# Performance work log

Measured on AMD Instinct MI355X. Metric: run time of the kernel, lower is better.

Reference implementation:

```python
import jax, jax.numpy as jnp
import numpy as np
from jax.ops import segment_sum

N_NODE, N_EDGE, D_IN, D_HID, N_CLS = 50000, 800000, 64, 64, 40


def setup_inputs() -> dict:
    key = jax.random.key(0)
    k1, k2, k3, k4 = jax.random.split(key, 4)
    x = jax.random.normal(k1, (N_NODE, D_IN), dtype=jnp.float32)
    edge_index = jax.random.randint(k2, (2, N_EDGE), 0, N_NODE, dtype=jnp.int64)
    W1 = jax.random.normal(k3, (D_IN, D_HID), dtype=jnp.float32) * (1.0 / np.sqrt(D_IN))
    b1 = jnp.zeros((D_HID,), dtype=jnp.float32)
    W2 = jax.random.normal(k4, (D_HID, N_CLS), dtype=jnp.float32) * (1.0 / np.sqrt(D_HID))
    b2 = jnp.zeros((N_CLS,), dtype=jnp.float32)
    return {"x": x, "edge_index": edge_index, "W1": W1, "b1": b1, "W2": W2, "b2": b2}


def _att_weights(fea, row, col, n):
    # edge-parallel cosine similarity (sklearn cosine_similarity restricted to edges)
    nrm = jnp.sqrt(jnp.sum(fea * fea, axis=1, keepdims=True))
    fn = fea / jnp.maximum(nrm, 1e-12)
    sim = jnp.sum(fn[row] * fn[col], axis=1)                 # [E]
    sim = jnp.where(sim < 0.1, 0.0, sim)                      # threshold
    # L1 row-normalization (sim >= 0 after threshold)
    rs = segment_sum(sim, row, num_segments=n)                # [N]
    sim_n = jnp.where(sim > 0, sim / jnp.maximum(rs[row], 1e-12), 0.0)
    # degree-based self-loop weight lam = 1/(deg+1)
    deg = segment_sum((sim > 0).astype(fea.dtype), row, num_segments=n)
    lam = 1.0 / (deg + 1.0)
    # exp applied only to stored (nonzero) entries; zeroed edges stay 0
    w_edge = jnp.where(sim > 0, jnp.exp(sim_n), 0.0)          # [E]
    w_self = jnp.exp(lam)                                     # [N] self-loop weights
    return w_edge, w_self


def _gcn(h, W, b, row, col, w_edge, w_self, n):
    # symmetric-norm GCN over weighted edges + explicit self loops
    deg = segment_sum(w_edge, row, num_segments=n) + w_self
    dinv = 1.0 / jnp.sqrt(jnp.maximum(deg, 1e-12))
    h = h @ W                                                 # [N, F]
    coef = w_edge * dinv[row] * dinv[col]                     # [E]
    out = segment_sum(coef[:, None] * h[col], row, num_segments=n)
    out = out + (w_self * dinv * dinv)[:, None] * h + b
    return out


def reference(x, edge_index, W1, b1, W2, b2):
    n = x.shape[0]
    row, col = edge_index[0], edge_index[1]
    # layer 1: attention coefs from raw features
    w1e, w1s = _att_weights(x, row, col, n)
    h = jax.nn.relu(_gcn(x, W1, b1, row, col, w1e, w1s, n))
    # layer 2: attention coefs recomputed on hidden features (dropout = eval mode)
    w2e, w2s = _att_weights(h, row, col, n)
    out = _gcn(h, W2, b2, row, col, w2e, w2s, n)
    return jax.nn.log_softmax(out, axis=1)
```

## Files before the change

### kernel.cpp

```cpp
#include <hip/hip_runtime.h>
#include <math.h>


#define ATT_CAP 96
#define EPB     2048
#define RPB     128
#define NBUCK_MAX 512
#define CAPB    4096

typedef _Float16 half4 __attribute__((ext_vector_type(4)));

__global__ void k_normfn(const float* __restrict__ fea, float* __restrict__ fn, int n)
{
    int gid  = blockIdx.x * blockDim.x + threadIdx.x;
    int wid  = gid >> 6;
    int lane = threadIdx.x & 63;
    if (wid >= n) return;
    float v = fea[(size_t)wid * 64 + lane];
    float s = v * v;
#pragma unroll
    for (int off = 32; off > 0; off >>= 1) s += __shfl_xor(s, off);
    float inv = 1.0f / fmaxf(sqrtf(s), 1e-12f);
    fn[(size_t)wid * 64 + lane] = v * inv;
}

__global__ void k_bhist(const int* __restrict__ row, int* __restrict__ hist,
                        int* __restrict__ btot, int E, int nblkA, int nbuck)
{
    __shared__ int lh[NBUCK_MAX];
    int b = blockIdx.x;
    int ebeg = b * EPB, eend = ebeg + EPB; if (eend > E) eend = E;
    for (int i = threadIdx.x; i < nbuck; i += blockDim.x) lh[i] = 0;
    __syncthreads();
    for (int e = ebeg + threadIdx.x; e < eend; e += blockDim.x)
        atomicAdd(&lh[row[e] >> 7], 1);
    __syncthreads();
    for (int i = threadIdx.x; i < nbuck; i += blockDim.x) {
        int c = lh[i];
        hist[(size_t)i * nblkA + b] = c;
        if (c) atomicAdd(btot + i, c);
    }
}

__global__ void k_bscan(const int* __restrict__ btot, int* __restrict__ bbase, int nbuck)
{
    int lane = threadIdx.x;
    int K = (nbuck + 63) / 64;
    int beg = lane * K;
    int s = 0;
    for (int i = 0; i < K; ++i) { int idx = beg + i; if (idx < nbuck) s += btot[idx]; }
    int incl = s;
#pragma unroll
    for (int off = 1; off < 64; off <<= 1) {
        int v = __shfl_up(incl, off);
        if (lane >= off) incl += v;
    }
    int run = incl - s;
    for (int i = 0; i < K; ++i) {
        int idx = beg + i;
        if (idx < nbuck) { bbase[idx] = run; run += btot[idx]; }
    }
    if (lane == 63) bbase[nbuck] = incl;
}

__global__ void k_mscan(int* __restrict__ hist, const int* __restrict__ bbase,
                        int nbuck, int nblkA)
{
    int wib  = threadIdx.x >> 6;
    int j    = blockIdx.x * 4 + wib;
    int lane = threadIdx.x & 63;
    if (j >= nbuck) return;
    int run = bbase[j];
    size_t base = (size_t)j * nblkA;
    for (int b0 = 0; b0 < nblkA; b0 += 64) {
        int b = b0 + lane;
        int v = (b < nblkA) ? hist[base + b] : 0;
        int incl = v;
#pragma unroll
        for (int off = 1; off < 64; off <<= 1) {
            int t = __shfl_up(incl, off);
            if (lane >= off) incl += t;
        }
        if (b < nblkA) hist[base + b] = run + (incl - v);
        run += __shfl(incl, 63);
    }
}

__global__ void k_bscat(const int* __restrict__ row, const int* __restrict__ col,
                        const int* __restrict__ hist, int* __restrict__ ebuf,
                        int E, int nblkA, int nbuck)
{
    __shared__ int lh[NBUCK_MAX];
    int b = blockIdx.x;
    int ebeg = b * EPB, eend = ebeg + EPB; if (eend > E) eend = E;
    for (int i = threadIdx.x; i < nbuck; i += blockDim.x)
        lh[i] = hist[(size_t)i * nblkA + b];
    __syncthreads();
    for (int e = ebeg + threadIdx.x; e < eend; e += blockDim.x) {
        int r = row[e];
        int j = r >> 7;
        int pos = atomicAdd(&lh[j], 1);
        ebuf[pos] = ((r & (RPB - 1)) << 16) | col[e];
    }
}

__global__ void k_csr(const int* __restrict__ ebuf, const int* __restrict__ bbase,
                      int* __restrict__ rptr, int* __restrict__ col_s, int N, int E)
{
    __shared__ int pk[CAPB];
    __shared__ int lcol[CAPB];
    __shared__ int lcnt[RPB], lexc[RPB], lcur[RPB];
    int j = blockIdx.x;
    int beg = bbase[j], end = bbase[j + 1];
    int m = end - beg; if (m > CAPB) m = CAPB;
    int tid = threadIdx.x;
    for (int i = tid; i < m; i += blockDim.x) pk[i] = ebuf[beg + i];
    if (tid < RPB) lcnt[tid] = 0;
    __syncthreads();
    for (int i = tid; i < m; i += blockDim.x) atomicAdd(&lcnt[pk[i] >> 16], 1);
    __syncthreads();
    if (tid < 64) {
        int a = lcnt[2 * tid], b2 = lcnt[2 * tid + 1];
        int s = a + b2;
        int incl = s;
#pragma unroll
        for (int off = 1; off < 64; off <<= 1) {
            int v = __shfl_up(incl, off);
            if (tid >= off) incl += v;
        }
        int base = incl - s;
        lexc[2 * tid] = base;     lexc[2 * tid + 1] = base + a;
        lcur[2 * tid] = base;     lcur[2 * tid + 1] = base + a;
    }
    __syncthreads();
    for (int i = tid; i < m; i += blockDim.x) {
        int v = pk[i];
        int p = atomicAdd(&lcur[v >> 16], 1);
        lcol[p] = v & 0xFFFF;
    }
    __syncthreads();
    for (int i = tid; i < m; i += blockDim.x) col_s[beg + i] = lcol[i];
    if (tid < RPB) {
        int r = j * RPB + tid;
        if (r < N) rptr[r] = beg + lexc[tid];
    }
    if (j == 0 && tid == 0) rptr[N] = E;
}

__global__ void k_att(const float* __restrict__ fn,
                      const int* __restrict__ rptr, const int* __restrict__ col_s,
                      int2* __restrict__ cw, int* __restrict__ lend,
                      float* __restrict__ dinv, float* __restrict__ selfc, int n)
{
    __shared__ float ssim[4][ATT_CAP];
    __shared__ int   scol[4][ATT_CAP];
    int wib  = threadIdx.x >> 6;
    int wid  = blockIdx.x * 4 + wib;
    int lane = threadIdx.x & 63;
    if (wid >= n) return;
    int sub = lane & 7;
    int grp = lane >> 3;
    int beg = rptr[wid], end = rptr[wid + 1];
    int deg_all = end - beg;

    const float4* frp = (const float4*)(fn + (size_t)wid * 64);
    float4 a0 = frp[sub * 2], a1 = frp[sub * 2 + 1];

    float rs_part = 0.0f;
    int ngrp = (deg_all + 7) >> 3;
    for (int g = 0; g < ngrp; ++g) {
        int li = g * 8 + grp;
        float s = 0.0f; int c = 0;
        bool valid = (li < deg_all);
        if (valid) {
            c = col_s[beg + li];
            const float4* fcp = (const float4*)(fn + (size_t)c * 64);
            float4 b0 = fcp[sub * 2], b1 = fcp[sub * 2 + 1];
            float p = a0.x * b0.x + a0.y * b0.y + a0.z * b0.z + a0.w * b0.w
                    + a1.x * b1.x + a1.y * b1.y + a1.z * b1.z + a1.w * b1.w;
            p += __shfl_xor(p, 1);
            p += __shfl_xor(p, 2);
            p += __shfl_xor(p, 4);
            s = (p < 0.1f) ? 0.0f : p;
        }
        if (sub == 0 && valid) {
            if (li < ATT_CAP) { ssim[wib][li] = s; scol[wib][li] = c; }
            if (s > 0.0f) rs_part += s;
        }
    }
#pragma unroll
    for (int off = 32; off > 0; off >>= 1) rs_part += __shfl_xor(rs_part, off);
    float denom = fmaxf(rs_part, 1e-12f);

    int   nlive = 0;
    float sw_lane = 0.0f;
    for (int base = 0; base < deg_all; base += 64) {
        int li = base + lane;
        bool valid = (li < deg_all);
        float s = 0.0f; int c = 0;
        if (valid) {
            if (li < ATT_CAP) { s = ssim[wib][li]; c = scol[wib][li]; }
            else {
                c = col_s[beg + li];
                const float* fr = fn + (size_t)wid * 64;
                const float* fc = fn + (size_t)c * 64;
                float p = 0.0f;
                for (int k = 0; k < 64; ++k) p += fr[k] * fc[k];
                s = (p < 0.1f) ? 0.0f : p;
            }
        }
        float w = (valid && s > 0.0f) ? expf(s / denom) : 0.0f;
        unsigned long long M = __ballot(w > 0.0f);
        int rank = __popcll(M & ((1ull << lane) - 1ull));
        if (w > 0.0f) {
            int2 pw; pw.x = c; pw.y = __float_as_int(w);
            cw[beg + nlive + rank] = pw;
            sw_lane += w;
        }
        nlive += __popcll(M);
    }
#pragma unroll
    for (int off = 32; off > 0; off >>= 1) sw_lane += __shfl_xor(sw_lane, off);

    if (lane == 0) {
        float wself = expf(1.0f / ((float)nlive + 1.0f));
        float D  = sw_lane + wself;
        float di = rsqrtf(fmaxf(D, 1e-12f));
        lend[wid]  = beg + nlive;
        dinv[wid]  = di;
        selfc[wid] = wself * di;
    }
}

template <int F, typename InT>
__global__ void k_gemm(const InT* __restrict__ fea, const float* __restrict__ W,
                       const float* __restrict__ scale, _Float16* __restrict__ out, int n)
{
    constexpr int R = 256 / F;
    __shared__ float sW[64 * F];
    __shared__ float sX[R * 64];
    int tid = threadIdx.x;
    for (int i = tid; i < 64 * F; i += 256) sW[i] = W[i];
    int base = blockIdx.x * R;
    for (int i = tid; i < R * 64; i += 256) {
        int rr = base + i / 64;
        sX[i] = (rr < n) ? (float)fea[(size_t)rr * 64 + (i & 63)] : 0.0f;
    }
    __syncthreads();
    int rl = tid / F, j = tid % F;
    if (rl >= R) return;
    int r = base + rl;
    if (r >= n) return;
    float acc = 0.0f;
#pragma unroll
    for (int k = 0; k < 64; ++k) acc = fmaf(sX[rl * 64 + k], sW[k * F + j], acc);
    out[(size_t)r * F + j] = (_Float16)(acc * scale[r]);
}

template <int F>
__device__ inline float agg_core_t(const _Float16* __restrict__ hd,
                                   const int2* __restrict__ cw,
                                   int beg, int lend_, int lane)
{
    int q  = lane & 15;
    int eg = lane >> 4;
    bool qact = (F == 64) ? true : (q < (F >> 2));
    float acc0 = 0.f, acc1 = 0.f, acc2 = 0.f, acc3 = 0.f;
    for (int base = beg; base < lend_; base += 64) {
        int idx = base + lane;
        int cv = 0; float wv = 0.0f;
        if (idx < lend_) { int2 pw = cw[idx]; cv = pw.x; wv = __int_as_float(pw.y); }
        int cnt = lend_ - base; if (cnt > 64) cnt = 64;
        for (int j = 0; j < cnt; j += 4) {
            int   c = __shfl(cv, j + eg);
            float w = __shfl(wv, j + eg);
            if (qact) {
                half4 hv = *(const half4*)(hd + (size_t)c * F + q * 4);
                acc0 += w * (float)hv.x;
                acc1 += w * (float)hv.y;
                acc2 += w * (float)hv.z;
                acc3 += w * (float)hv.w;
            }
        }
    }
    acc0 += __shfl_xor(acc0, 16); acc0 += __shfl_xor(acc0, 32);
    acc1 += __shfl_xor(acc1, 16); acc1 += __shfl_xor(acc1, 32);
    acc2 += __shfl_xor(acc2, 16); acc2 += __shfl_xor(acc2, 32);
    acc3 += __shfl_xor(acc3, 16); acc3 += __shfl_xor(acc3, 32);
    int srcq = lane >> 2;
    float a0 = __shfl(acc0, srcq);
    float a1 = __shfl(acc1, srcq);
    float a2 = __shfl(acc2, srcq);
    float a3 = __shfl(acc3, srcq);
    int k = lane & 3;
    return (k == 0) ? a0 : (k == 1) ? a1 : (k == 2) ? a2 : a3;
}

__global__ void k_agg64(const _Float16* __restrict__ hd, const int2* __restrict__ cw,
                        const float* __restrict__ dinv, const float* __restrict__ selfc,
                        const float* __restrict__ b, const int* __restrict__ row_ptr,
                        const int* __restrict__ lend,
                        _Float16* __restrict__ hrelu16, float* __restrict__ fnh, int n)
{
    int gid  = blockIdx.x * blockDim.x + threadIdx.x;
    int wid  = gid >> 6;
    int lane = threadIdx.x & 63;
    if (wid >= n) return;
    int beg = row_ptr[wid], le = lend[wid];
    float accf = agg_core_t<64>(hd, cw, beg, le, lane);
    float hs  = (float)hd[(size_t)wid * 64 + lane];
    float v = dinv[wid] * accf + selfc[wid] * hs + b[lane];
    v = fmaxf(v, 0.0f);
    hrelu16[(size_t)wid * 64 + lane] = (_Float16)v;
    float s = v * v;
#pragma unroll
    for (int off = 32; off > 0; off >>= 1) s += __shfl_xor(s, off);
    float inv = 1.0f / fmaxf(sqrtf(s), 1e-12f);
    fnh[(size_t)wid * 64 + lane] = v * inv;
}

__global__ void k_agg40_lsm(const _Float16* __restrict__ hd2, const int2* __restrict__ cw,
                            const float* __restrict__ dinv, const float* __restrict__ selfc,
                            const float* __restrict__ b, const int* __restrict__ row_ptr,
                            const int* __restrict__ lend,
                            float* __restrict__ out, int n)
{
    constexpr int F = 40;
    int gid  = blockIdx.x * blockDim.x + threadIdx.x;
    int wid  = gid >> 6;
    int lane = threadIdx.x & 63;
    if (wid >= n) return;
    int beg = row_ptr[wid], le = lend[wid];
    float accf = agg_core_t<F>(hd2, cw, beg, le, lane);
    bool active = (lane < F);
    float v = 0.0f;
    if (active) {
        float hs = (float)hd2[(size_t)wid * F + lane];
        v = dinv[wid] * accf + selfc[wid] * hs + b[lane];
    }
    float m = active ? v : -__builtin_inff();
#pragma unroll
    for (int off = 32; off > 0; off >>= 1) m = fmaxf(m, __shfl_xor(m, off));
    float ex = active ? expf(v - m) : 0.0f;
    float s = ex;
#pragma unroll
    for (int off = 32; off > 0; off >>= 1) s += __shfl_xor(s, off);
    if (active) out[(size_t)wid * F + lane] = v - m - logf(s);
}

extern "C" void kernel_launch(void* const* d_in, const int* in_sizes, int n_in,
                              void* d_out, int out_size, void* d_ws, size_t ws_size,
                              hipStream_t stream)
{
    const float* x  = (const float*)d_in[0];
    const int*   ei = (const int*)d_in[1];
    const float* W1 = (const float*)d_in[2];
    const float* b1 = (const float*)d_in[3];
    const float* W2 = (const float*)d_in[4];
    const float* b2 = (const float*)d_in[5];
    float* out = (float*)d_out;

    const int N = in_sizes[0] / 64;
    const int E = in_sizes[1] / 2;
    const int* row = ei;
    const int* col = ei + E;

    const int nblkA = (E + EPB - 1) / EPB;
    const int nbuck = (N + RPB - 1) / RPB;

    char* p = (char*)d_ws;
    auto alloc = [&](size_t bytes) -> char* {
        char* r = p; p += (bytes + 255) & ~(size_t)255; return r;
    };
    float*     fn     = (float*)alloc((size_t)N * 64 * 4);
    float*     dinv   = (float*)alloc((size_t)N * 4);
    float*     selfc  = (float*)alloc((size_t)N * 4);
    _Float16*  hd1    = (_Float16*)alloc((size_t)N * 64 * 2);
    _Float16*  hrelu  = (_Float16*)alloc((size_t)N * 64 * 2);
    _Float16*  hd2    = (_Float16*)alloc((size_t)N * 40 * 2);
    float*     fnh    = (float*)alloc((size_t)N * 64 * 4);
    int*       rptr   = (int*)alloc((size_t)(N + 1) * 4);
    int*       lendv  = (int*)alloc((size_t)N * 4);
    int*       col_s  = (int*)alloc((size_t)E * 4);
    int2*      cw     = (int2*)alloc((size_t)E * 8);
    int*       ebuf   = (int*)alloc((size_t)E * 4);
    int*       hist   = (int*)alloc((size_t)nbuck * nblkA * 4);
    int*       btot   = (int*)alloc((size_t)nbuck * 4);
    int*       bbase  = (int*)alloc((size_t)(nbuck + 1) * 4);

    const int TB = 256;
    int blk_nodeWave = (N * 64 + TB - 1) / TB;
    int blk_node4    = (N + 3) / 4;

    hipMemsetAsync(btot, 0, (size_t)nbuck * 4, stream);

    k_bhist<<<nblkA, TB, 0, stream>>>(row, hist, btot, E, nblkA, nbuck);
    k_bscan<<<1, 64, 0, stream>>>(btot, bbase, nbuck);
    k_mscan<<<(nbuck + 3) / 4, TB, 0, stream>>>(hist, bbase, nbuck, nblkA);
    k_bscat<<<nblkA, TB, 0, stream>>>(row, col, hist, ebuf, E, nblkA, nbuck);
    k_csr<<<nbuck, TB, 0, stream>>>(ebuf, bbase, rptr, col_s, N, E);

    k_normfn<<<blk_nodeWave, TB, 0, stream>>>(x, fn, N);
    k_att<<<blk_node4, TB, 0, stream>>>(fn, rptr, col_s, cw, lendv, dinv, selfc, N);
    k_gemm<64, float><<<(N + 3) / 4, TB, 0, stream>>>(x, W1, dinv, hd1, N);
    k_agg64<<<blk_nodeWave, TB, 0, stream>>>(hd1, cw, dinv, selfc, b1,
                                             rptr, lendv, hrelu, fnh, N);

    k_att<<<blk_node4, TB, 0, stream>>>(fnh, rptr, col_s, cw, lendv, dinv, selfc, N);
    k_gemm<40, _Float16><<<(N + 5) / 6, TB, 0, stream>>>(hrelu, W2, dinv, hd2, N);
    k_agg40_lsm<<<blk_nodeWave, TB, 0, stream>>>(hd2, cw, dinv, selfc, b2,
                                                 rptr, lendv, out, N);
}
```

Before: 285.5 us.

## Replace per-block histogram scan with atomic bucket cursors; store layer-1 features in fp32

The bucket sort no longer writes a per-block histogram matrix and drops the multi-block scan kernel. Each scatter block now counts its edges locally, reserves a contiguous range per bucket with one global atomicAdd on a cursor array, and writes its edges in a second pass from registers. This removes one kernel launch and the histogram traffic, at the cost of a nondeterministic edge order inside each bucket, which the CSR pass later sorts by row. Separately, the layer-1 transformed features are now kept in fp32 rather than fp16. That doubles the gather bytes in the first aggregation but removes the fp16 conversion error.

```diff
diff --git a/kernel.cpp b/kernel.cpp
--- a/kernel.cpp
+++ b/kernel.cpp
@@ -24,8 +24,8 @@
     fn[(size_t)wid * 64 + lane] = v * inv;
 }
 
-__global__ void k_bhist(const int* __restrict__ row, int* __restrict__ hist,
-                        int* __restrict__ btot, int E, int nblkA, int nbuck)
+__global__ void k_bhist(const int* __restrict__ row, int* __restrict__ btot,
+                        int E, int nbuck)
 {
     __shared__ int lh[NBUCK_MAX];
     int b = blockIdx.x;
@@ -35,14 +35,12 @@
     for (int e = ebeg + threadIdx.x; e < eend; e += blockDim.x)
         atomicAdd(&lh[row[e] >> 7], 1);
     __syncthreads();
-    for (int i = threadIdx.x; i < nbuck; i += blockDim.x) {
-        int c = lh[i];
-        hist[(size_t)i * nblkA + b] = c;
-        if (c) atomicAdd(btot + i, c);
-    }
-}
-
-__global__ void k_bscan(const int* __restrict__ btot, int* __restrict__ bbase, int nbuck)
+    for (int i = threadIdx.x; i < nbuck; i += blockDim.x)
+        if (lh[i]) atomicAdd(btot + i, lh[i]);
+}
+
+__global__ void k_bscan(const int* __restrict__ btot, int* __restrict__ bbase,
+                        int* __restrict__ gcur, int nbuck)
 {
     int lane = threadIdx.x;
     int K = (nbuck + 63) / 64;
@@ -58,49 +56,38 @@
     int run = incl - s;
     for (int i = 0; i < K; ++i) {
         int idx = beg + i;
-        if (idx < nbuck) { bbase[idx] = run; run += btot[idx]; }
+        if (idx < nbuck) { bbase[idx] = run; gcur[idx] = run; run += btot[idx]; }
     }
     if (lane == 63) bbase[nbuck] = incl;
 }
 
-__global__ void k_mscan(int* __restrict__ hist, const int* __restrict__ bbase,
-                        int nbuck, int nblkA)
-{
-    int wib  = threadIdx.x >> 6;
-    int j    = blockIdx.x * 4 + wib;
-    int lane = threadIdx.x & 63;
-    if (j >= nbuck) return;
-    int run = bbase[j];
-    size_t base = (size_t)j * nblkA;
-    for (int b0 = 0; b0 < nblkA; b0 += 64) {
-        int b = b0 + lane;
-        int v = (b < nblkA) ? hist[base + b] : 0;
-        int incl = v;
-#pragma unroll
-        for (int off = 1; off < 64; off <<= 1) {
-            int t = __shfl_up(incl, off);
-            if (lane >= off) incl += t;
-        }
-        if (b < nblkA) hist[base + b] = run + (incl - v);
-        run += __shfl(incl, 63);
-    }
-}
-
 __global__ void k_bscat(const int* __restrict__ row, const int* __restrict__ col,
-                        const int* __restrict__ hist, int* __restrict__ ebuf,
-                        int E, int nblkA, int nbuck)
+                        int* __restrict__ gcur, int* __restrict__ ebuf, int E, int nbuck)
 {
     __shared__ int lh[NBUCK_MAX];
+    __shared__ int lbase[NBUCK_MAX];
     int b = blockIdx.x;
     int ebeg = b * EPB, eend = ebeg + EPB; if (eend > E) eend = E;
-    for (int i = threadIdx.x; i < nbuck; i += blockDim.x)
-        lh[i] = hist[(size_t)i * nblkA + b];
+    int rr[8], cc[8];
+    int ne = 0;
+    for (int i = threadIdx.x; i < nbuck; i += blockDim.x) lh[i] = 0;
     __syncthreads();
     for (int e = ebeg + threadIdx.x; e < eend; e += blockDim.x) {
-        int r = row[e];
-        int j = r >> 7;
-        int pos = atomicAdd(&lh[j], 1);
-        ebuf[pos] = ((r & (RPB - 1)) << 16) | col[e];
+        int r = row[e], c = col[e];
+        rr[ne] = r; cc[ne] = c; ++ne;
+        atomicAdd(&lh[r >> 7], 1);
+    }
+    __syncthreads();
+    for (int i = threadIdx.x; i < nbuck; i += blockDim.x) {
+        int cnt = lh[i];
+        if (cnt) lbase[i] = atomicAdd(gcur + i, cnt);
+        lh[i] = 0;
+    }
+    __syncthreads();
+    for (int k = 0; k < ne; ++k) {
+        int j = rr[k] >> 7;
+        int pos = lbase[j] + atomicAdd(&lh[j], 1);
+        ebuf[pos] = ((rr[k] & (RPB - 1)) << 16) | cc[k];
     }
 }
 
@@ -232,9 +219,9 @@
     }
 }
 
-template <int F, typename InT>
+template <int F, typename InT, typename OutT>
 __global__ void k_gemm(const InT* __restrict__ fea, const float* __restrict__ W,
-                       const float* __restrict__ scale, _Float16* __restrict__ out, int n)
+                       const float* __restrict__ scale, OutT* __restrict__ out, int n)
 {
     constexpr int R = 256 / F;
     __shared__ float sW[64 * F];
@@ -254,11 +241,11 @@
     float acc = 0.0f;
 #pragma unroll
     for (int k = 0; k < 64; ++k) acc = fmaf(sX[rl * 64 + k], sW[k * F + j], acc);
-    out[(size_t)r * F + j] = (_Float16)(acc * scale[r]);
-}
-
-template <int F>
-__device__ inline float agg_core_t(const _Float16* __restrict__ hd,
+    out[(size_t)r * F + j] = (OutT)(acc * scale[r]);
+}
+
+template <int F, typename Vec4>
+__device__ inline float agg_core_t(const Vec4* __restrict__ hdv,
                                    const int2* __restrict__ cw,
                                    int beg, int lend_, int lane)
 {
@@ -275,7 +262,7 @@
             int   c = __shfl(cv, j + eg);
             float w = __shfl(wv, j + eg);
             if (qact) {
-                half4 hv = *(const half4*)(hd + (size_t)c * F + q * 4);
+                Vec4 hv = hdv[(size_t)c * (F >> 2) + q];
                 acc0 += w * (float)hv.x;
                 acc1 += w * (float)hv.y;
                 acc2 += w * (float)hv.z;
@@ -296,7 +283,7 @@
     return (k == 0) ? a0 : (k == 1) ? a1 : (k == 2) ? a2 : a3;
 }
 
-__global__ void k_agg64(const _Float16* __restrict__ hd, const int2* __restrict__ cw,
+__global__ void k_agg64(const float* __restrict__ hd, const int2* __restrict__ cw,
                         const float* __restrict__ dinv, const float* __restrict__ selfc,
                         const float* __restrict__ b, const int* __restrict__ row_ptr,
                         const int* __restrict__ lend,
@@ -307,8 +294,8 @@
     int lane = threadIdx.x & 63;
     if (wid >= n) return;
     int beg = row_ptr[wid], le = lend[wid];
-    float accf = agg_core_t<64>(hd, cw, beg, le, lane);
-    float hs  = (float)hd[(size_t)wid * 64 + lane];
+    float accf = agg_core_t<64>((const float4*)hd, cw, beg, le, lane);
+    float hs  = hd[(size_t)wid * 64 + lane];
     float v = dinv[wid] * accf + selfc[wid] * hs + b[lane];
     v = fmaxf(v, 0.0f);
     hrelu16[(size_t)wid * 64 + lane] = (_Float16)v;
@@ -331,7 +318,7 @@
     int lane = threadIdx.x & 63;
     if (wid >= n) return;
     int beg = row_ptr[wid], le = lend[wid];
-    float accf = agg_core_t<F>(hd2, cw, beg, le, lane);
+    float accf = agg_core_t<F>((const half4*)hd2, cw, beg, le, lane);
     bool active = (lane < F);
     float v = 0.0f;
     if (active) {
@@ -375,7 +362,7 @@
     float*     fn     = (float*)alloc((size_t)N * 64 * 4);
     float*     dinv   = (float*)alloc((size_t)N * 4);
     float*     selfc  = (float*)alloc((size_t)N * 4);
-    _Float16*  hd1    = (_Float16*)alloc((size_t)N * 64 * 2);
+    float*     hd1    = (float*)alloc((size_t)N * 64 * 4);
     _Float16*  hrelu  = (_Float16*)alloc((size_t)N * 64 * 2);
     _Float16*  hd2    = (_Float16*)alloc((size_t)N * 40 * 2);
     float*     fnh    = (float*)alloc((size_t)N * 64 * 4);
@@ -384,9 +371,9 @@
     int*       col_s  = (int*)alloc((size_t)E * 4);
     int2*      cw     = (int2*)alloc((size_t)E * 8);
     int*       ebuf   = (int*)alloc((size_t)E * 4);
-    int*       hist   = (int*)alloc((size_t)nbuck * nblkA * 4);
     int*       btot   = (int*)alloc((size_t)nbuck * 4);
     int*       bbase  = (int*)alloc((size_t)(nbuck + 1) * 4);
+    int*       gcur   = (int*)alloc((size_t)nbuck * 4);
 
     const int TB = 256;
     int blk_nodeWave = (N * 64 + TB - 1) / TB;
@@ -394,20 +381,19 @@
 
     hipMemsetAsync(btot, 0, (size_t)nbuck * 4, stream);
 
-    k_bhist<<<nblkA, TB, 0, stream>>>(row, hist, btot, E, nblkA, nbuck);
-    k_bscan<<<1, 64, 0, stream>>>(btot, bbase, nbuck);
-    k_mscan<<<(nbuck + 3) / 4, TB, 0, stream>>>(hist, bbase, nbuck, nblkA);
-    k_bscat<<<nblkA, TB, 0, stream>>>(row, col, hist, ebuf, E, nblkA, nbuck);
+    k_bhist<<<nblkA, TB, 0, stream>>>(row, btot, E, nbuck);
+    k_bscan<<<1, 64, 0, stream>>>(btot, bbase, gcur, nbuck);
+    k_bscat<<<nblkA, TB, 0, stream>>>(row, col, gcur, ebuf, E, nbuck);
     k_csr<<<nbuck, TB, 0, stream>>>(ebuf, bbase, rptr, col_s, N, E);
 
     k_normfn<<<blk_nodeWave, TB, 0, stream>>>(x, fn, N);
     k_att<<<blk_node4, TB, 0, stream>>>(fn, rptr, col_s, cw, lendv, dinv, selfc, N);
-    k_gemm<64, float><<<(N + 3) / 4, TB, 0, stream>>>(x, W1, dinv, hd1, N);
+    k_gemm<64, float, float><<<(N + 3) / 4, TB, 0, stream>>>(x, W1, dinv, hd1, N);
     k_agg64<<<blk_nodeWave, TB, 0, stream>>>(hd1, cw, dinv, selfc, b1,
                                              rptr, lendv, hrelu, fnh, N);
 
     k_att<<<blk_node4, TB, 0, stream>>>(fnh, rptr, col_s, cw, lendv, dinv, selfc, N);
-    k_gemm<40, _Float16><<<(N + 5) / 6, TB, 0, stream>>>(hrelu, W2, dinv, hd2, N);
+    k_gemm<40, _Float16, _Float16><<<(N + 5) / 6, TB, 0, stream>>>(hrelu, W2, dinv, hd2, N);
     k_agg40_lsm<<<blk_nodeWave, TB, 0, stream>>>(hd2, cw, dinv, selfc, b2,
                                                  rptr, lendv, out, N);
 }
```

After: 286.8 us. No clear change (+0.4%).
